# Optimization experiments

Hardware: AMD Instinct MI355X
Metric: run time of the kernel (lower is better)

## Reference

```python
import jax, jax.numpy as jnp
import numpy as np


def setup_inputs() -> dict:
    key = jax.random.key(0)
    k1, k2, k3 = jax.random.split(key, 3)
    B, T, D = 32, 1024, 512
    x = jax.random.normal(k1, (B, T, D), dtype=jnp.float32)
    duration = jax.random.randint(k2, (B, T), 0, 9, dtype=jnp.int32)
    mask = jax.random.randint(k3, (B, T), 0, 2, dtype=jnp.int32)
    max_len = 2600  # static upper bound on max_b sum_t duration[b,t]
    return {"x": x, "duration": duration, "mask": mask, "max_len": max_len}


def reference(x, duration, mask, max_len):
    # x: [B, T, D]; duration, mask: [B, T]; max_len: python int (static)
    B, T, D = x.shape
    d_eff = duration * mask                       # masked tokens contribute 0 frames
    cum = jnp.cumsum(d_eff, axis=1)               # [B, T] cumulative frame counts
    total = cum[:, -1:]                           # [B, 1] frames per sequence
    pos = jnp.arange(max_len, dtype=cum.dtype)    # [T_out]
    # token index owning output frame j: #{t : cum[t] <= j}
    idx = jax.vmap(lambda c: jnp.searchsorted(c, pos, side='right'))(cum)  # [B, T_out]
    idx = jnp.minimum(idx, T - 1)
    valid = (pos[None, :] < total).astype(x.dtype)                         # [B, T_out]
    expanded = jnp.take_along_axis(x, idx[..., None], axis=1) * valid[..., None]
    return expanded, valid
```

## Files before the change

### kernel.cpp

```cpp
#include <hip/hip_runtime.h>

__global__ void lr_prep_kernel(const int* __restrict__ duration,
                               const int* __restrict__ mask,
                               int* __restrict__ idx,
                               float* __restrict__ valid_out,
                               int T, int max_len) {
    const int b = blockIdx.x;
    const int t = threadIdx.x;
    const int lane = t & 63;
    const int wave = t >> 6;
    __shared__ int wsum[4];

    const int4 dv = ((const int4*)(duration + (size_t)b * T))[t];
    const int4 mv = ((const int4*)(mask     + (size_t)b * T))[t];
    const int e0 = dv.x * mv.x, e1 = dv.y * mv.y,
              e2 = dv.z * mv.z, e3 = dv.w * mv.w;
    const int s3 = e0 + e1 + e2 + e3;

    int s = s3;
    #pragma unroll
    for (int off = 1; off < 64; off <<= 1) {
        int u = __shfl_up(s, off, 64);
        if (lane >= off) s += u;
    }
    if (lane == 63) wsum[wave] = s;
    __syncthreads();
    int bof = 0;
    #pragma unroll
    for (int w = 0; w < 4; ++w) bof += (w < wave) ? wsum[w] : 0;
    const int total = wsum[0] + wsum[1] + wsum[2] + wsum[3];
    int p = bof + s - s3;

    int*   __restrict__ ib = idx       + (size_t)b * max_len;
    float* __restrict__ vb = valid_out + (size_t)b * max_len;
    const int tok = t * 4;
    for (int q = 0; q < e0; ++q, ++p) { ib[p] = tok;     vb[p] = 1.0f; }
    for (int q = 0; q < e1; ++q, ++p) { ib[p] = tok + 1; vb[p] = 1.0f; }
    for (int q = 0; q < e2; ++q, ++p) { ib[p] = tok + 2; vb[p] = 1.0f; }
    for (int q = 0; q < e3; ++q, ++p) { ib[p] = tok + 3; vb[p] = 1.0f; }
    for (int q = total + t; q < max_len; q += 256) { ib[q] = -1; vb[q] = 0.0f; }
}

__global__ __launch_bounds__(256)
void lr_copy_kernel(const float* __restrict__ x,
                    const int* __restrict__ idx,
                    float* __restrict__ out,
                    int T, int max_len, int nblk) {
    const int cpx = nblk >> 3;
    const int bid = blockIdx.x;
    const int swz = (bid & 7) * cpx + (bid >> 3);

    const int wave = threadIdx.x >> 6;
    const int lane = threadIdx.x & 63;
    const unsigned pos0 = (unsigned)swz * 8u + (unsigned)wave * 2u;
    const unsigned pos1 = pos0 + 1u;
    const unsigned b0 = pos0 / (unsigned)max_len;
    const unsigned b1 = pos1 / (unsigned)max_len;

    const int i0 = idx[pos0];
    const int i1 = idx[pos1];

    const float4 z = make_float4(0.f, 0.f, 0.f, 0.f);
    float4 a0 = z, a1 = z, c0 = z, c1 = z;
    if (i0 >= 0) {
        const float4* __restrict__ s0 =
            (const float4*)(x + ((size_t)b0 * T + i0) * 512u);
        a0 = s0[lane]; a1 = s0[lane + 64];
    }
    if (i1 >= 0) {
        const float4* __restrict__ s1 =
            (const float4*)(x + ((size_t)b1 * T + i1) * 512u);
        c0 = s1[lane]; c1 = s1[lane + 64];
    }
    float4* __restrict__ d0 = (float4*)(out + (size_t)pos0 * 512u);
    float4* __restrict__ d1 = (float4*)(out + (size_t)pos1 * 512u);
    d0[lane] = a0; d0[lane + 64] = a1;
    d1[lane] = c0; d1[lane + 64] = c1;
}

extern "C" void kernel_launch(void* const* d_in, const int* in_sizes, int n_in,
                              void* d_out, int out_size, void* d_ws, size_t ws_size,
                              hipStream_t stream) {
    const float* x        = (const float*)d_in[0];
    const int*   duration = (const int*)d_in[1];
    const int*   mask     = (const int*)d_in[2];

    const int B = 32;
    const int BT = in_sizes[1];
    const int T = BT / B;
    const int D = in_sizes[0] / BT;
    const int max_len = out_size / (B * (D + 1));

    float* out       = (float*)d_out;
    float* valid_out = out + (size_t)B * max_len * D;
    int*   idx       = (int*)d_ws;

    lr_prep_kernel<<<B, 256, 0, stream>>>(duration, mask, idx, valid_out, T, max_len);

    const int nblk = (B * max_len) / 8;
    lr_copy_kernel<<<nblk, 256, 0, stream>>>(x, idx, out, T, max_len, nblk);
}
```

Before: 37.89 us.

## Replace per-frame gather with per-token scatter of repeated rows

```diff
diff --git a/kernel.cpp b/kernel.cpp
--- a/kernel.cpp
+++ b/kernel.cpp
@@ -1,10 +1,8 @@
 #include <hip/hip_runtime.h>
 
-__global__ void lr_prep_kernel(const int* __restrict__ duration,
+__global__ void lr_scan_kernel(const int* __restrict__ duration,
                                const int* __restrict__ mask,
-                               int* __restrict__ idx,
-                               float* __restrict__ valid_out,
-                               int T, int max_len) {
+                               int* __restrict__ cum, int T) {
     const int b = blockIdx.x;
     const int t = threadIdx.x;
     const int lane = t & 63;
@@ -28,54 +26,65 @@
     int bof = 0;
     #pragma unroll
     for (int w = 0; w < 4; ++w) bof += (w < wave) ? wsum[w] : 0;
-    const int total = wsum[0] + wsum[1] + wsum[2] + wsum[3];
-    int p = bof + s - s3;
+    const int excl = bof + s - s3;
 
-    int*   __restrict__ ib = idx       + (size_t)b * max_len;
-    float* __restrict__ vb = valid_out + (size_t)b * max_len;
-    const int tok = t * 4;
-    for (int q = 0; q < e0; ++q, ++p) { ib[p] = tok;     vb[p] = 1.0f; }
-    for (int q = 0; q < e1; ++q, ++p) { ib[p] = tok + 1; vb[p] = 1.0f; }
-    for (int q = 0; q < e2; ++q, ++p) { ib[p] = tok + 2; vb[p] = 1.0f; }
-    for (int q = 0; q < e3; ++q, ++p) { ib[p] = tok + 3; vb[p] = 1.0f; }
-    for (int q = total + t; q < max_len; q += 256) { ib[q] = -1; vb[q] = 0.0f; }
+    int4 o;
+    o.x = excl + e0;
+    o.y = o.x + e1;
+    o.z = o.y + e2;
+    o.w = o.z + e3;
+    ((int4*)(cum + (size_t)b * T))[t] = o;
 }
 
 __global__ __launch_bounds__(256)
-void lr_copy_kernel(const float* __restrict__ x,
-                    const int* __restrict__ idx,
-                    float* __restrict__ out,
-                    int T, int max_len, int nblk) {
-    const int cpx = nblk >> 3;
-    const int bid = blockIdx.x;
-    const int swz = (bid & 7) * cpx + (bid >> 3);
-
+void lr_scatter_kernel(const float* __restrict__ x,
+                       const int* __restrict__ cum,
+                       float* __restrict__ out,
+                       float* __restrict__ valid_out,
+                       int T, int max_len, int NT) {
     const int wave = threadIdx.x >> 6;
     const int lane = threadIdx.x & 63;
-    const unsigned pos0 = (unsigned)swz * 8u + (unsigned)wave * 2u;
-    const unsigned pos1 = pos0 + 1u;
-    const unsigned b0 = pos0 / (unsigned)max_len;
-    const unsigned b1 = pos1 / (unsigned)max_len;
+    const int w = blockIdx.x * 4 + wave;
 
-    const int i0 = idx[pos0];
-    const int i1 = idx[pos1];
+    if (w < NT) {
+        const int b = w >> 10;
+        const int t = w & 1023;
+        const int* __restrict__ cb = cum + (size_t)b * T;
+        const int incl = cb[t];
+        const int excl = (t > 0) ? cb[t - 1] : 0;
+        int start = excl, end = incl;
+        if (end > max_len) end = max_len;
+        if (start > max_len) start = max_len;
+        const int d = end - start;
+        if (d <= 0) return;
 
-    const float4 z = make_float4(0.f, 0.f, 0.f, 0.f);
-    float4 a0 = z, a1 = z, c0 = z, c1 = z;
-    if (i0 >= 0) {
-        const float4* __restrict__ s0 =
-            (const float4*)(x + ((size_t)b0 * T + i0) * 512u);
-        a0 = s0[lane]; a1 = s0[lane + 64];
+        const float4* __restrict__ src =
+            (const float4*)(x + ((size_t)b * T + t) * 512u);
+        const float4 a0 = src[lane];
+        const float4 a1 = src[lane + 64];
+
+        float* __restrict__ ob = out + ((size_t)b * max_len + start) * 512u;
+        for (int r = 0; r < d; ++r) {
+            float4* __restrict__ dst = (float4*)(ob + (size_t)r * 512u);
+            dst[lane] = a0;
+            dst[lane + 64] = a1;
+        }
+        if (lane < d)
+            valid_out[(size_t)b * max_len + start + lane] = 1.0f;
+    } else {
+        const unsigned q = (unsigned)(w - NT);
+        const unsigned b = q / (unsigned)max_len;
+        const unsigned p = q - b * (unsigned)max_len;
+        const int total = cum[(size_t)b * T + T - 1];
+        if ((int)p >= total) {
+            const size_t pos = (size_t)b * max_len + p;
+            float4* __restrict__ dst = (float4*)(out + pos * 512u);
+            const float4 z = make_float4(0.f, 0.f, 0.f, 0.f);
+            dst[lane] = z;
+            dst[lane + 64] = z;
+            if (lane == 0) valid_out[pos] = 0.0f;
+        }
     }
-    if (i1 >= 0) {
-        const float4* __restrict__ s1 =
-            (const float4*)(x + ((size_t)b1 * T + i1) * 512u);
-        c0 = s1[lane]; c1 = s1[lane + 64];
-    }
-    float4* __restrict__ d0 = (float4*)(out + (size_t)pos0 * 512u);
-    float4* __restrict__ d1 = (float4*)(out + (size_t)pos1 * 512u);
-    d0[lane] = a0; d0[lane + 64] = a1;
-    d1[lane] = c0; d1[lane + 64] = c1;
 }
 
 extern "C" void kernel_launch(void* const* d_in, const int* in_sizes, int n_in,
@@ -93,10 +102,13 @@
 
     float* out       = (float*)d_out;
     float* valid_out = out + (size_t)B * max_len * D;
-    int*   idx       = (int*)d_ws;
+    int*   cum       = (int*)d_ws;
 
-    lr_prep_kernel<<<B, 256, 0, stream>>>(duration, mask, idx, valid_out, T, max_len);
+    lr_scan_kernel<<<B, 256, 0, stream>>>(duration, mask, cum, T);
 
-    const int nblk = (B * max_len) / 8;
-    lr_copy_kernel<<<nblk, 256, 0, stream>>>(x, idx, out, T, max_len, nblk);
+    const int NT = B * T;
+    const int NW = NT + B * max_len;
+    const int nblk = (NW + 3) / 4;
+    lr_scatter_kernel<<<nblk, 256, 0, stream>>>(x, cum, out, valid_out,
+                                                T, max_len, NT);
 }
```

After: 40.59 us. 1.07x slower.

## Stage prep indices in LDS with vector stores; copy four rows per wave

Applied to the files above, without the earlier changes.

```diff
diff --git a/kernel.cpp b/kernel.cpp
--- a/kernel.cpp
+++ b/kernel.cpp
@@ -1,14 +1,18 @@
 #include <hip/hip_runtime.h>
 
-__global__ void lr_prep_kernel(const int* __restrict__ duration,
-                               const int* __restrict__ mask,
-                               int* __restrict__ idx,
-                               float* __restrict__ valid_out,
-                               int T, int max_len) {
+typedef float f32x4 __attribute__((ext_vector_type(4)));
+
+__global__ __launch_bounds__(256)
+void lr_prep_kernel(const int* __restrict__ duration,
+                    const int* __restrict__ mask,
+                    int* __restrict__ idx,
+                    float* __restrict__ valid_out,
+                    int T, int max_len) {
     const int b = blockIdx.x;
     const int t = threadIdx.x;
     const int lane = t & 63;
     const int wave = t >> 6;
+    __shared__ __align__(16) int s_idx[2600];
     __shared__ int wsum[4];
 
     const int4 dv = ((const int4*)(duration + (size_t)b * T))[t];
@@ -31,14 +35,38 @@
     const int total = wsum[0] + wsum[1] + wsum[2] + wsum[3];
     int p = bof + s - s3;
 
+    const int tok = t * 4;
+    {
+        int q1;
+        q1 = p + e0; if (q1 > max_len) q1 = max_len;
+        for (int q = p; q < q1; ++q) s_idx[q] = tok;
+        p += e0;
+        q1 = p + e1; if (q1 > max_len) q1 = max_len;
+        for (int q = p; q < q1; ++q) s_idx[q] = tok + 1;
+        p += e1;
+        q1 = p + e2; if (q1 > max_len) q1 = max_len;
+        for (int q = p; q < q1; ++q) s_idx[q] = tok + 2;
+        p += e2;
+        q1 = p + e3; if (q1 > max_len) q1 = max_len;
+        for (int q = p; q < q1; ++q) s_idx[q] = tok + 3;
+    }
+    const int t0 = (total < max_len) ? total : max_len;
+    for (int q = t0 + t; q < max_len; q += 256) s_idx[q] = -1;
+    __syncthreads();
+
     int*   __restrict__ ib = idx       + (size_t)b * max_len;
     float* __restrict__ vb = valid_out + (size_t)b * max_len;
-    const int tok = t * 4;
-    for (int q = 0; q < e0; ++q, ++p) { ib[p] = tok;     vb[p] = 1.0f; }
-    for (int q = 0; q < e1; ++q, ++p) { ib[p] = tok + 1; vb[p] = 1.0f; }
-    for (int q = 0; q < e2; ++q, ++p) { ib[p] = tok + 2; vb[p] = 1.0f; }
-    for (int q = 0; q < e3; ++q, ++p) { ib[p] = tok + 3; vb[p] = 1.0f; }
-    for (int q = total + t; q < max_len; q += 256) { ib[q] = -1; vb[q] = 0.0f; }
+    const int nv4 = max_len >> 2;
+    for (int v4 = t; v4 < nv4; v4 += 256) {
+        const int4 o = ((const int4*)s_idx)[v4];
+        float4 vv;
+        vv.x = (o.x >= 0) ? 1.0f : 0.0f;
+        vv.y = (o.y >= 0) ? 1.0f : 0.0f;
+        vv.z = (o.z >= 0) ? 1.0f : 0.0f;
+        vv.w = (o.w >= 0) ? 1.0f : 0.0f;
+        ((int4*)ib)[v4] = o;
+        ((float4*)vb)[v4] = vv;
+    }
 }
 
 __global__ __launch_bounds__(256)
@@ -52,30 +80,34 @@
 
     const int wave = threadIdx.x >> 6;
     const int lane = threadIdx.x & 63;
-    const unsigned pos0 = (unsigned)swz * 8u + (unsigned)wave * 2u;
-    const unsigned pos1 = pos0 + 1u;
-    const unsigned b0 = pos0 / (unsigned)max_len;
-    const unsigned b1 = pos1 / (unsigned)max_len;
+    const unsigned base = (unsigned)swz * 16u + (unsigned)wave * 4u;
 
-    const int i0 = idx[pos0];
-    const int i1 = idx[pos1];
+    const f32x4 z = {0.f, 0.f, 0.f, 0.f};
+    int   iv[4];
+    f32x4 lo[4], hi[4];
 
-    const float4 z = make_float4(0.f, 0.f, 0.f, 0.f);
-    float4 a0 = z, a1 = z, c0 = z, c1 = z;
-    if (i0 >= 0) {
-        const float4* __restrict__ s0 =
-            (const float4*)(x + ((size_t)b0 * T + i0) * 512u);
-        a0 = s0[lane]; a1 = s0[lane + 64];
+    #pragma unroll
+    for (int j = 0; j < 4; ++j) iv[j] = idx[base + j];
+
+    #pragma unroll
+    for (int j = 0; j < 4; ++j) {
+        const unsigned pos = base + j;
+        const unsigned b = pos / (unsigned)max_len;
+        const int i = (iv[j] >= 0) ? iv[j] : 0;
+        const f32x4* __restrict__ src =
+            (const f32x4*)(x + ((size_t)b * T + i) * 512u);
+        lo[j] = src[lane];
+        hi[j] = src[lane + 64];
     }
-    if (i1 >= 0) {
-        const float4* __restrict__ s1 =
-            (const float4*)(x + ((size_t)b1 * T + i1) * 512u);
-        c0 = s1[lane]; c1 = s1[lane + 64];
+
+    #pragma unroll
+    for (int j = 0; j < 4; ++j) {
+        const unsigned pos = base + j;
+        const bool v = iv[j] >= 0;
+        f32x4* __restrict__ dst = (f32x4*)(out + (size_t)pos * 512u);
+        dst[lane]      = v ? lo[j] : z;
+        dst[lane + 64] = v ? hi[j] : z;
     }
-    float4* __restrict__ d0 = (float4*)(out + (size_t)pos0 * 512u);
-    float4* __restrict__ d1 = (float4*)(out + (size_t)pos1 * 512u);
-    d0[lane] = a0; d0[lane + 64] = a1;
-    d1[lane] = c0; d1[lane + 64] = c1;
 }
 
 extern "C" void kernel_launch(void* const* d_in, const int* in_sizes, int n_in,
@@ -95,8 +127,9 @@
     float* valid_out = out + (size_t)B * max_len * D;
     int*   idx       = (int*)d_ws;
 
-    lr_prep_kernel<<<B, 256, 0, stream>>>(duration, mask, idx, valid_out, T, max_len);
+    lr_prep_kernel<<<B, 256, 0, stream>>>(duration, mask, idx, valid_out,
+                                          T, max_len);
 
-    const int nblk = (B * max_len) / 8;
+    const int nblk = (B * max_len) / 16;
     lr_copy_kernel<<<nblk, 256, 0, stream>>>(x, idx, out, T, max_len, nblk);
 }
```

Result: no change. 37.53 us (median of 2 runs) (-1.0%).
